# Performance work log

Hardware: AMD Instinct MI355X
Metric: run time of the kernel (lower is better)

Reference implementation:

```python
import jax, jax.numpy as jnp
import numpy as np

B, S, D = 4, 2048, 1024
H, K = 16, 64
EPS = 1e-3  # Keras LayerNormalization default epsilon


def setup_inputs() -> dict:
    key = jax.random.key(0)
    ks = jax.random.split(key, 11)
    s = 0.02
    return {
        "x":  jax.random.normal(ks[0], (B, S, D), jnp.float32),
        "Wq": jax.random.normal(ks[1], (D, H, K), jnp.float32) * s,
        "bq": jnp.zeros((H, K), jnp.float32),
        "Wk": jax.random.normal(ks[2], (D, H, K), jnp.float32) * s,
        "bk": jnp.zeros((H, K), jnp.float32),
        "Wv": jax.random.normal(ks[3], (D, H, K), jnp.float32) * s,
        "bv": jnp.zeros((H, K), jnp.float32),
        "Wo": jax.random.normal(ks[4], (H, K, D), jnp.float32) * s,
        "bo": jnp.zeros((D,), jnp.float32),
        "gamma": jnp.ones((D,), jnp.float32),
        "beta":  jnp.zeros((D,), jnp.float32),
    }


def reference(x, Wq, bq, Wk, bk, Wv, bv, Wo, bo, gamma, beta):
    # QKV projections (Keras MHA einsum form): [B,S,D] -> [B,S,H,K]
    q = jnp.einsum("bsd,dhk->bshk", x, Wq) + bq
    k = jnp.einsum("bsd,dhk->bshk", x, Wk) + bk
    v = jnp.einsum("bsd,dhk->bshk", x, Wv) + bv
    scale = 1.0 / jnp.sqrt(jnp.asarray(K, x.dtype))
    scores = jnp.einsum("bqhk,bshk->bhqs", q, k) * scale  # [B,H,S,S]
    attn = jax.nn.softmax(scores, axis=-1)
    ctx = jnp.einsum("bhqs,bshk->bqhk", attn, v)           # [B,S,H,K]
    attn_out = jnp.einsum("bqhk,hkd->bqd", ctx, Wo) + bo   # [B,S,D]
    # residual + LayerNorm (over last axis)
    y = x + attn_out
    mu = jnp.mean(y, axis=-1, keepdims=True)
    var = jnp.mean(jnp.square(y - mu), axis=-1, keepdims=True)
    return (y - mu) * jax.lax.rsqrt(var + EPS) * gamma + beta
```

## Files before the change

kernel.cpp:

```cpp
#include <hip/hip_runtime.h>

typedef float f32x4 __attribute__((ext_vector_type(4)));
typedef float f32x16 __attribute__((ext_vector_type(16)));
typedef __bf16 bf16x8 __attribute__((ext_vector_type(8)));
typedef __bf16 bf16x4 __attribute__((ext_vector_type(4)));
typedef __bf16 bf16x2 __attribute__((ext_vector_type(2)));
typedef unsigned short us4 __attribute__((ext_vector_type(4)));

#define DEV __device__ __forceinline__

DEV unsigned short f2bf(float f) {
  union { float f; unsigned int u; } v; v.f = f;
  unsigned int u = v.u;
  return (unsigned short)((u + 0x7FFFu + ((u >> 16) & 1u)) >> 16);
}

typedef const __attribute__((address_space(1))) void* gvp;
typedef __attribute__((address_space(3))) void* lvp;

DEV void gll16(const void* g, void* l) {
  __builtin_amdgcn_global_load_lds((gvp)g, (lvp)l, 16, 0, 0);
}

DEV float fexp2(float x) { return __builtin_amdgcn_exp2f(x); }

DEV void plswap(unsigned& a, unsigned& b) {
  asm("v_permlane32_swap_b32 %0, %1" : "+v"(a), "+v"(b));
}
DEV float xhalf_sum(float v) {
  union { float f; unsigned u; } a, b;
  a.f = v; b.f = v;
  plswap(a.u, b.u);
  return a.f + b.f;
}

__global__ void k_pre(const float* __restrict__ x, unsigned short* __restrict__ xb,
                      const float* __restrict__ w0, const float* __restrict__ w1,
                      const float* __restrict__ w2, const float* __restrict__ w3,
                      unsigned short* __restrict__ o0, unsigned short* __restrict__ o1,
                      unsigned short* __restrict__ o2, unsigned short* __restrict__ o3) {
  __shared__ float tile[32][33];
  const int bid = blockIdx.x;
  const int tid = threadIdx.x;
  if (bid < 8192) {
    int i = bid * 256 + tid;
    float4 v = ((const float4*)x)[i];
    us4 o = { f2bf(v.x), f2bf(v.y), f2bf(v.z), f2bf(v.w) };
    ((us4*)xb)[i] = o;
    return;
  }
  int t = bid - 8192;
  const int z = t >> 10;
  t &= 1023;
  const float* in = (z == 0) ? w0 : (z == 1) ? w1 : (z == 2) ? w2 : w3;
  unsigned short* out = (z == 0) ? o0 : (z == 1) ? o1 : (z == 2) ? o2 : o3;
  const int bx = (t & 31) * 32, by = (t >> 5) * 32;
  const int tx = tid & 31, ty = tid >> 5;
#pragma unroll
  for (int r = 0; r < 4; ++r)
    tile[ty + r * 8][tx] = in[(size_t)(by + ty + r * 8) * 1024 + bx + tx];
  __syncthreads();
#pragma unroll
  for (int r = 0; r < 4; ++r)
    out[(size_t)(bx + ty + r * 8) * 1024 + by + tx] = f2bf(tile[tx][ty + r * 8]);
}

__global__ void k_gemm_qkv(const unsigned short* __restrict__ xb,
                           const unsigned short* __restrict__ wqt,
                           const unsigned short* __restrict__ wkt,
                           const unsigned short* __restrict__ wvt,
                           const float* __restrict__ bq, const float* __restrict__ bk,
                           const float* __restrict__ bv,
                           unsigned short* __restrict__ qb, unsigned short* __restrict__ kb,
                           unsigned short* __restrict__ vtb) {
  __shared__ unsigned short SM[2][128 * 64];
  unsigned short* As = SM[0];
  unsigned short* Bs = SM[1];
  const int tid = threadIdx.x;
  const int lane = tid & 63;
  const int wave = tid >> 6;
  const int l15 = lane & 15;
  const int lq  = lane >> 4;
  const int wm = wave >> 1, wn = wave & 1;
  const int z = blockIdx.z;

  const unsigned short* A;
  const unsigned short* Bt;
  int mbase, nbase;
  if (z == 2) { A = wvt; Bt = xb; mbase = blockIdx.y * 128; nbase = blockIdx.x * 128; }
  else        { A = xb; Bt = z ? wkt : wqt; mbase = blockIdx.x * 128; nbase = blockIdx.y * 128; }

  f32x4 acc[4][4] = {};

  for (int kt = 0; kt < 1024; kt += 64) {
    __syncthreads();
#pragma unroll
    for (int c = 0; c < 4; ++c) {
      int e = (c * 256 + tid) * 8;
      int row = e >> 6;
      int o2 = (e * 2) ^ ((row & 7) << 4);
      int col = (o2 >> 1) & 63;
      gll16(A + (size_t)(mbase + row) * 1024 + kt + col,
            As + (c * 256 + (tid & ~63)) * 8);
      gll16(Bt + (size_t)(nbase + row) * 1024 + kt + col,
            Bs + (c * 256 + (tid & ~63)) * 8);
    }
    __syncthreads();
#pragma unroll
    for (int ks = 0; ks < 2; ++ks) {
      bf16x8 af[4], bfv[4];
#pragma unroll
      for (int i = 0; i < 4; ++i) {
        int row = wm * 64 + i * 16 + l15;
        int off = row * 128 + ((((ks << 2) | lq) ^ (row & 7)) << 4);
        af[i] = *(const bf16x8*)((const char*)As + off);
      }
#pragma unroll
      for (int j = 0; j < 4; ++j) {
        int row = wn * 64 + j * 16 + l15;
        int off = row * 128 + ((((ks << 2) | lq) ^ (row & 7)) << 4);
        bfv[j] = *(const bf16x8*)((const char*)Bs + off);
      }
#pragma unroll
      for (int i = 0; i < 4; ++i)
#pragma unroll
        for (int j = 0; j < 4; ++j)
          acc[i][j] = __builtin_amdgcn_mfma_f32_16x16x32_bf16(bfv[j], af[i], acc[i][j], 0, 0, 0);
    }
  }

  const float scale = (z == 0) ? 0.18033688011112042f : 1.0f;
  const float* bias = (z == 0) ? bq : (z == 1) ? bk : bv;
  unsigned short* outp = (z == 0) ? qb : (z == 1) ? kb : vtb;

  float4 bj[4];
  if (z < 2) {
#pragma unroll
    for (int j = 0; j < 4; ++j)
      bj[j] = *(const float4*)&bias[nbase + wn * 64 + j * 16 + lq * 4];
  }

  __syncthreads();
  char* T = (char*)SM;
#pragma unroll
  for (int i = 0; i < 4; ++i) {
    const int miL = wm * 64 + i * 16 + l15;
    const int sw = (miL & 7) << 4;
    const float bm = (z == 2) ? bias[mbase + miL] : 0.f;
#pragma unroll
    for (int j = 0; j < 4; ++j) {
      const int nj2 = (wn * 64 + j * 16 + lq * 4) * 2;
      bf16x4 p;
#pragma unroll
      for (int r = 0; r < 4; ++r) {
        float v = acc[i][j][r];
        v = (z < 2) ? (v + ((const float*)&bj[j])[r]) * scale : (v + bm);
        p[r] = (__bf16)v;
      }
      *(bf16x4*)(T + miL * 256 + (nj2 ^ sw)) = p;
    }
  }
  __syncthreads();

#pragma unroll
  for (int c = 0; c < 8; ++c) {
    const int lin = c * 256 + tid;
    const int row = lin >> 4;
    const int s16 = lin & 15;
    bf16x8 vv = *(const bf16x8*)(T + row * 256 + ((s16 * 16) ^ ((row & 7) << 4)));
    const int mi = mbase + row;
    const int nj = nbase + s16 * 8;
    size_t gaddr;
    if (z < 2) {
      gaddr = (((size_t)((mi >> 11) * 16 + (nj >> 6)) * 2048 + (mi & 2047)) << 6) + (nj & 63);
    } else {
      gaddr = ((size_t)(((nj >> 11) * 16 + (mi >> 6)) * 64 + (mi & 63))) * 2048 + (nj & 2047);
    }
    *(bf16x8*)(outp + gaddr) = vv;
  }
}

__global__ void k_gemm_out(const unsigned short* __restrict__ A,
                           const unsigned short* __restrict__ Bt,
                           const float* __restrict__ bias,
                           unsigned short* __restrict__ yb,
                           const unsigned short* __restrict__ xres) {
  __shared__ unsigned short SM[2][128 * 64];
  unsigned short* As = SM[0];
  unsigned short* Bs = SM[1];
  const int tid = threadIdx.x;
  const int lane = tid & 63;
  const int wave = tid >> 6;
  const int l15 = lane & 15;
  const int lq  = lane >> 4;
  const int wm = wave >> 1, wn = wave & 1;
  const int mbase = blockIdx.x * 128;
  const int nbase = blockIdx.y * 128;

  f32x4 acc[4][4] = {};

  for (int kt = 0; kt < 1024; kt += 64) {
    __syncthreads();
#pragma unroll
    for (int c = 0; c < 4; ++c) {
      int e = (c * 256 + tid) * 8;
      int row = e >> 6;
      int o2 = (e * 2) ^ ((row & 7) << 4);
      int col = (o2 >> 1) & 63;
      gll16(A + (size_t)(mbase + row) * 1024 + kt + col,
            As + (c * 256 + (tid & ~63)) * 8);
      gll16(Bt + (size_t)(nbase + row) * 1024 + kt + col,
            Bs + (c * 256 + (tid & ~63)) * 8);
    }
    __syncthreads();
#pragma unroll
    for (int ks = 0; ks < 2; ++ks) {
      bf16x8 af[4], bfv[4];
#pragma unroll
      for (int i = 0; i < 4; ++i) {
        int row = wm * 64 + i * 16 + l15;
        int off = row * 128 + ((((ks << 2) | lq) ^ (row & 7)) << 4);
        af[i] = *(const bf16x8*)((const char*)As + off);
      }
#pragma unroll
      for (int j = 0; j < 4; ++j) {
        int row = wn * 64 + j * 16 + l15;
        int off = row * 128 + ((((ks << 2) | lq) ^ (row & 7)) << 4);
        bfv[j] = *(const bf16x8*)((const char*)Bs + off);
      }
#pragma unroll
      for (int i = 0; i < 4; ++i)
#pragma unroll
        for (int j = 0; j < 4; ++j)
          acc[i][j] = __builtin_amdgcn_mfma_f32_16x16x32_bf16(bfv[j], af[i], acc[i][j], 0, 0, 0);
    }
  }

  float4 bj[4];
#pragma unroll
  for (int j = 0; j < 4; ++j)
    bj[j] = *(const float4*)&bias[nbase + wn * 64 + j * 16 + lq * 4];

  __syncthreads();
  char* T = (char*)SM;
#pragma unroll
  for (int i = 0; i < 4; ++i) {
    const int miL = wm * 64 + i * 16 + l15;
    const int sw = (miL & 7) << 4;
#pragma unroll
    for (int j = 0; j < 4; ++j) {
      const int nj2 = (wn * 64 + j * 16 + lq * 4) * 2;
      bf16x4 p;
#pragma unroll
      for (int r = 0; r < 4; ++r)
        p[r] = (__bf16)(acc[i][j][r] + ((const float*)&bj[j])[r]);
      *(bf16x4*)(T + miL * 256 + (nj2 ^ sw)) = p;
    }
  }
  __syncthreads();

#pragma unroll
  for (int c = 0; c < 8; ++c) {
    const int lin = c * 256 + tid;
    const int row = lin >> 4;
    const int s16 = lin & 15;
    bf16x8 vv = *(const bf16x8*)(T + row * 256 + ((s16 * 16) ^ ((row & 7) << 4)));
    const size_t g = (size_t)(mbase + row) * 1024 + nbase + s16 * 8;
    bf16x8 xv = *(const bf16x8*)(xres + g);
    bf16x8 ov;
#pragma unroll
    for (int e = 0; e < 8; ++e)
      ov[e] = (__bf16)((float)vv[e] + (float)xv[e]);
    *(bf16x8*)(yb + g) = ov;
  }
}

__global__ __launch_bounds__(256, 4) void k_attn(const unsigned short* __restrict__ q,
                       const unsigned short* __restrict__ k,
                       const unsigned short* __restrict__ vt,
                       unsigned short* __restrict__ ctx) {
  __shared__ unsigned short KV[2][2][64 * 64];

  const int tid = threadIdx.x;
  const int lane = tid & 63;
  const int wave = tid >> 6;
  const int l31 = lane & 31;
  const int l5 = lane >> 5;
  const int prl = l31 >> 1;
  const int b3  = (l31 & 1) << 3;

  const int bid = blockIdx.x;
  const int swz = (bid & 7) * 128 + (bid >> 3);
  const int bh = swz >> 4;
  const int qtile = swz & 15;
  const int qbase = qtile * 128;
  const size_t sl = (size_t)bh << 17;

  const int qrow = qbase + wave * 32 + l31;
  bf16x8 qreg[4];
#pragma unroll
  for (int ds = 0; ds < 4; ++ds)
    qreg[ds] = *(const bf16x8*)(q + sl + (size_t)qrow * 64 + ds * 16 + l5 * 8);

#define STAGE_KV(BUF, TT) do {                                                 \
    const int kvb_ = (TT) * 64;                                                \
    _Pragma("unroll")                                                          \
    for (int c = 0; c < 2; ++c) {                                              \
      int ci = c * 256 + tid;                                                  \
      int pr_ = ci >> 4;                                                       \
      int u_ = (ci & 15) ^ (pr_ & 15);                                         \
      int lrow_ = pr_ * 2 + (u_ >> 3);                                         \
      int lc_ = u_ & 7;                                                        \
      gll16(k + sl + (size_t)(kvb_ + lrow_) * 64 + lc_ * 8,                    \
            KV[BUF][0] + (c * 256 + (tid & ~63)) * 8);                         \
      gll16(vt + sl + (size_t)lrow_ * 2048 + kvb_ + lc_ * 8,                   \
            KV[BUF][1] + (c * 256 + (tid & ~63)) * 8);                         \
    }                                                                          \
  } while (0)

  STAGE_KV(0, 0);
  __syncthreads();

  f32x16 acc0 = {}, acc1 = {};
  float lrow = 0.f;

  for (int t = 0; t < 32; ++t) {
    const int cur = t & 1;
    if (t < 31) STAGE_KV(cur ^ 1, t + 1);

    const char* Ksc = (const char*)KV[cur][0];
    const char* Vtc = (const char*)KV[cur][1];

    bf16x8 kf0[4], kf1[4];
#pragma unroll
    for (int ds = 0; ds < 4; ++ds) {
      int sc = (b3 | (2 * ds + l5)) ^ prl;
      kf0[ds] = *(const bf16x8*)(Ksc + prl * 256 + sc * 16);
      kf1[ds] = *(const bf16x8*)(Ksc + 4096 + prl * 256 + sc * 16);
    }
    f32x16 s0 = {}, s1 = {};
    __builtin_amdgcn_s_setprio(1);
#pragma unroll
    for (int ds = 0; ds < 4; ++ds)
      s0 = __builtin_amdgcn_mfma_f32_32x32x16_bf16(kf0[ds], qreg[ds], s0, 0, 0, 0);
#pragma unroll
    for (int ds = 0; ds < 4; ++ds)
      s1 = __builtin_amdgcn_mfma_f32_32x32x16_bf16(kf1[ds], qreg[ds], s1, 0, 0, 0);
    __builtin_amdgcn_s_setprio(0);
    __builtin_amdgcn_sched_barrier(0);

    unsigned pk0[8], pk1[8];
    float r0s = 0.f, r1s = 0.f, r2s = 0.f, r3s = 0.f;
#pragma unroll
    for (int m = 0; m < 8; ++m) {
      float a0 = fexp2(s0[2 * m]), a1 = fexp2(s0[2 * m + 1]);
      float b0 = fexp2(s1[2 * m]), b1 = fexp2(s1[2 * m + 1]);
      r0s += a0; r1s += a1; r2s += b0; r3s += b1;
      union { bf16x2 v; unsigned u; } ua, ub;
      ua.v = bf16x2{ (__bf16)a0, (__bf16)a1 };
      ub.v = bf16x2{ (__bf16)b0, (__bf16)b1 };
      pk0[m] = ua.u; pk1[m] = ub.u;
    }
    lrow += (r0s + r1s) + (r2s + r3s);
    __builtin_amdgcn_sched_barrier(0);

    bf16x8 av0[4], av1[4];
#pragma unroll
    for (int kvg = 0; kvg < 4; ++kvg) {
      int sc = (b3 | (2 * kvg + l5)) ^ prl;
      av0[kvg] = *(const bf16x8*)(Vtc + prl * 256 + sc * 16);
      av1[kvg] = *(const bf16x8*)(Vtc + 4096 + prl * 256 + sc * 16);
    }
    __builtin_amdgcn_s_setprio(1);
#pragma unroll
    for (int kvh = 0; kvh < 2; ++kvh) {
      unsigned* pk = kvh ? pk1 : pk0;
#pragma unroll
      for (int g = 0; g < 2; ++g) {
        unsigned a0_ = pk[4 * g],     b0_ = pk[4 * g + 2];
        unsigned a1_ = pk[4 * g + 1], b1_ = pk[4 * g + 3];
        plswap(a0_, b0_);
        plswap(a1_, b1_);
        union { unsigned u[4]; bf16x8 v; } pf;
        pf.u[0] = a0_; pf.u[1] = a1_; pf.u[2] = b0_; pf.u[3] = b1_;
        const int kvg = 2 * kvh + g;
        acc0 = __builtin_amdgcn_mfma_f32_32x32x16_bf16(av0[kvg], pf.v, acc0, 0, 0, 0);
        acc1 = __builtin_amdgcn_mfma_f32_32x32x16_bf16(av1[kvg], pf.v, acc1, 0, 0, 0);
      }
    }
    __builtin_amdgcn_s_setprio(0);

    __syncthreads();
  }

  const float inv = 1.f / xhalf_sum(lrow);

  unsigned short* TR = (unsigned short*)KV;
  const int qloc = wave * 32 + l31;
  const int swq = (qloc & 7) << 4;
#pragma unroll
  for (int dh = 0; dh < 2; ++dh) {
    const f32x16& ac = dh ? acc1 : acc0;
#pragma unroll
    for (int g3 = 0; g3 < 4; ++g3) {
      bf16x4 o4 = { (__bf16)(ac[4 * g3] * inv), (__bf16)(ac[4 * g3 + 1] * inv),
                    (__bf16)(ac[4 * g3 + 2] * inv), (__bf16)(ac[4 * g3 + 3] * inv) };
      *(bf16x4*)((char*)TR + qloc * 128 + ((dh * 64 + g3 * 16 + l5 * 8) ^ swq)) = o4;
    }
  }
  __syncthreads();

  const int b = bh >> 4, h = bh & 15;
  {
    int row = tid >> 1, half = tid & 1;
    int sw = (row & 7) << 4;
    unsigned short* gdst = ctx + (size_t)(b * 2048 + qbase + row) * 1024 + h * 64 + half * 32;
#pragma unroll
    for (int i = 0; i < 4; ++i) {
      bf16x8 vv = *(const bf16x8*)((const char*)TR + row * 128 + ((half * 64 + i * 16) ^ sw));
      *(bf16x8*)(gdst + i * 8) = vv;
    }
  }
#undef STAGE_KV
}

__global__ void k_ln(const unsigned short* __restrict__ y, const float* __restrict__ gamma,
                     const float* __restrict__ beta, float* __restrict__ out) {
  const int row = blockIdx.x;
  const int tid = threadIdx.x;
  const bf16x4 v4 = *(const bf16x4*)(y + (size_t)row * 1024 + tid * 4);
  float v0 = (float)v4[0], v1 = (float)v4[1], v2 = (float)v4[2], v3 = (float)v4[3];
  float sum = v0 + v1 + v2 + v3;
  float sq = v0 * v0 + v1 * v1 + v2 * v2 + v3 * v3;
#pragma unroll
  for (int m = 1; m <= 32; m <<= 1) {
    sum += __shfl_xor(sum, m);
    sq  += __shfl_xor(sq, m);
  }
  __shared__ float s1[4], s2[4];
  const int wv = tid >> 6, lane = tid & 63;
  if (lane == 0) { s1[wv] = sum; s2[wv] = sq; }
  __syncthreads();
  sum = s1[0] + s1[1] + s1[2] + s1[3];
  sq  = s2[0] + s2[1] + s2[2] + s2[3];
  const float mu = sum * (1.f / 1024.f);
  const float rs = rsqrtf(sq * (1.f / 1024.f) - mu * mu + 1e-3f);
  const float4 g  = ((const float4*)gamma)[tid];
  const float4 bb = ((const float4*)beta)[tid];
  float4 o;
  o.x = (v0 - mu) * rs * g.x + bb.x;
  o.y = (v1 - mu) * rs * g.y + bb.y;
  o.z = (v2 - mu) * rs * g.z + bb.z;
  o.w = (v3 - mu) * rs * g.w + bb.w;
  ((float4*)(out + (size_t)row * 1024))[tid] = o;
}

extern "C" void kernel_launch(void* const* d_in, const int* in_sizes, int n_in,
                              void* d_out, int out_size, void* d_ws, size_t ws_size,
                              hipStream_t stream) {
  const float* x  = (const float*)d_in[0];
  const float* Wq = (const float*)d_in[1];
  const float* bq = (const float*)d_in[2];
  const float* Wk = (const float*)d_in[3];
  const float* bk = (const float*)d_in[4];
  const float* Wv = (const float*)d_in[5];
  const float* bv = (const float*)d_in[6];
  const float* Wo = (const float*)d_in[7];
  const float* bo = (const float*)d_in[8];
  const float* gamma = (const float*)d_in[9];
  const float* beta  = (const float*)d_in[10];
  float* out = (float*)d_out;

  char* ws = (char*)d_ws;
  const size_t MB = 1024 * 1024;
  unsigned short* xb  = (unsigned short*)(ws);
  unsigned short* wqt = (unsigned short*)(ws + 16 * MB);
  unsigned short* wkt = (unsigned short*)(ws + 18 * MB);
  unsigned short* wvt = (unsigned short*)(ws + 20 * MB);
  unsigned short* wot = (unsigned short*)(ws + 22 * MB);
  unsigned short* qb  = (unsigned short*)(ws + 24 * MB);
  unsigned short* kb  = (unsigned short*)(ws + 40 * MB);
  unsigned short* vtb = (unsigned short*)(ws + 56 * MB);
  unsigned short* ctx = (unsigned short*)(ws + 72 * MB);
  unsigned short* yb  = (unsigned short*)(ws + 24 * MB);

  k_pre<<<12288, 256, 0, stream>>>(x, xb, Wq, Wk, Wv, Wo, wqt, wkt, wvt, wot);

  k_gemm_qkv<<<dim3(64, 8, 3), 256, 0, stream>>>(xb, wqt, wkt, wvt, bq, bk, bv, qb, kb, vtb);

  k_attn<<<1024, 256, 0, stream>>>(qb, kb, vtb, ctx);

  k_gemm_out<<<dim3(64, 8), 256, 0, stream>>>(ctx, wot, bo, yb, xb);

  k_ln<<<8192, 256, 0, stream>>>(yb, gamma, beta, out);
  (void)in_sizes; (void)n_in; (void)out_size; (void)ws_size;
}
```

Before: 175.2 us.

## Split Q/K projection into 256x256 eight-wave pipelined GEMM, keep separate V kernel

Replaces the combined QKV GEMM with a dedicated Q/K kernel using 256x256 tiles, 512 threads and a hand-scheduled double-buffered global_load_lds pipeline. It relies on explicit vmcnt waits, sched barriers and setprio around the MFMA bursts. The Wq and Wk weights are treated as one contiguous 2048-wide B matrix. V is computed by a separate smaller kernel using the old tiling. The aim is higher data reuse per tile and overlapping loads with MFMA work. The cost is fragile manual wait counts and only one block per CU.

After: 179.0 us. +2.2%, slower.

```diff
diff --git a/kernel.cpp b/kernel.cpp
--- a/kernel.cpp
+++ b/kernel.cpp
@@ -65,30 +65,181 @@
     out[(size_t)(bx + ty + r * 8) * 1024 + by + tx] = f2bf(tile[tx][ty + r * 8]);
 }
 
-__global__ void k_gemm_qkv(const unsigned short* __restrict__ xb,
-                           const unsigned short* __restrict__ wqt,
-                           const unsigned short* __restrict__ wkt,
-                           const unsigned short* __restrict__ wvt,
-                           const float* __restrict__ bq, const float* __restrict__ bk,
-                           const float* __restrict__ bv,
-                           unsigned short* __restrict__ qb, unsigned short* __restrict__ kb,
-                           unsigned short* __restrict__ vtb) {
-  __shared__ unsigned short SM[2][128 * 64];
-  unsigned short* As = SM[0];
-  unsigned short* Bs = SM[1];
+__global__ __launch_bounds__(512, 1) void k_gemm8_qk(
+    const unsigned short* __restrict__ A,
+    const unsigned short* __restrict__ Bt,
+    const float* __restrict__ bq, const float* __restrict__ bk,
+    unsigned short* __restrict__ qb, unsigned short* __restrict__ kb) {
+  __shared__ unsigned short SM[65536];
+  const int tid = threadIdx.x;
+  const int lane = tid & 63;
+  const int wave = tid >> 6;
+  const int l15 = lane & 15;
+  const int lq = lane >> 4;
+  const int wm = wave >> 2;
+  const int wn = wave & 3;
+
+  const int lin = blockIdx.x;
+  const int swz = (lin & 7) * 32 + (lin >> 3);
+  const int mt = swz & 31, nt = swz >> 5;
+  const int mbase = mt * 256, nbase = nt * 256;
+  const int z = nt >> 2;
+
+  const int sgrow = tid >> 3;
+  const int sgo2 = ((tid & 7) * 16) ^ ((sgrow & 7) << 4);
+  const int sgcol = sgo2 >> 1;
+  const int sdst = (tid & ~63) * 8;
+
+#define SQA(PAR, HALF, S, T) \
+  gll16(A + (size_t)(mbase + (HALF) * 128 + (S) * 64 + sgrow) * 1024 + (T) * 64 + sgcol, \
+        SM + (PAR) * 16384 + (HALF) * 8192 + (S) * 4096 + sdst)
+#define SQB(PAR, HALF, S, T) \
+  gll16(Bt + (size_t)(nbase + (HALF) * 128 + (S) * 64 + sgrow) * 1024 + (T) * 64 + sgcol, \
+        SM + 32768 + (PAR) * 16384 + (HALF) * 8192 + (S) * 4096 + sdst)
+#define SLOT_Aq(PAR, S, T) do { SQA(PAR, 0, S, T); SQA(PAR, 1, S, T); } while (0)
+#define SLOT_Bq(PAR, S, T) do { SQB(PAR, 0, S, T); SQB(PAR, 1, S, T); } while (0)
+
+  f32x4 acc[8][4] = {};
+  bf16x8 afr[4][2], bfr[2][2];
+
+  const char* Ab0 = (const char*)(SM + wm * 8192);
+  const char* Ab1 = (const char*)(SM + 16384 + wm * 8192);
+  const char* Bb0 = (const char*)(SM + 32768 + (wn >> 1) * 8192);
+  const char* Bb1 = (const char*)(SM + 49152 + (wn >> 1) * 8192);
+
+#define PHASE(ABASE, BBASE, MH, NH, LOADA, WAITSTMT, STAGESTMT) do {           \
+    WAITSTMT;                                                                  \
+    __builtin_amdgcn_s_barrier();                                              \
+    __builtin_amdgcn_sched_barrier(0);                                         \
+    if (LOADA) {                                                               \
+      _Pragma("unroll")                                                        \
+      for (int i = 0; i < 4; ++i) {                                            \
+        int lr = (MH) * 64 + i * 16 + l15;                                     \
+        _Pragma("unroll")                                                      \
+        for (int ks = 0; ks < 2; ++ks)                                         \
+          afr[i][ks] = *(const bf16x8*)((ABASE) + lr * 128 +                   \
+                        ((((ks << 2) | lq) ^ (lr & 7)) << 4));                 \
+      }                                                                        \
+    }                                                                          \
+    _Pragma("unroll")                                                          \
+    for (int j = 0; j < 2; ++j) {                                              \
+      int br = (wn & 1) * 64 + (NH) * 32 + j * 16 + l15;                       \
+      _Pragma("unroll")                                                        \
+      for (int ks = 0; ks < 2; ++ks)                                           \
+        bfr[j][ks] = *(const bf16x8*)((BBASE) + br * 128 +                     \
+                      ((((ks << 2) | lq) ^ (br & 7)) << 4));                   \
+    }                                                                          \
+    STAGESTMT;                                                                 \
+    asm volatile("s_waitcnt lgkmcnt(0)" ::: "memory");                         \
+    __builtin_amdgcn_sched_barrier(0);                                         \
+    __builtin_amdgcn_s_setprio(1);                                             \
+    _Pragma("unroll")                                                          \
+    for (int i = 0; i < 4; ++i)                                                \
+      _Pragma("unroll")                                                        \
+      for (int j = 0; j < 2; ++j)                                              \
+        _Pragma("unroll")                                                      \
+        for (int ks = 0; ks < 2; ++ks)                                         \
+          acc[(MH) * 4 + i][(NH) * 2 + j] =                                    \
+            __builtin_amdgcn_mfma_f32_16x16x32_bf16(bfr[j][ks], afr[i][ks],    \
+                acc[(MH) * 4 + i][(NH) * 2 + j], 0, 0, 0);                     \
+    __builtin_amdgcn_s_setprio(0);                                             \
+  } while (0)
+
+#define VM4 asm volatile("s_waitcnt vmcnt(4)" ::: "memory")
+#define VM6 asm volatile("s_waitcnt vmcnt(6)" ::: "memory")
+#define VM8 asm volatile("s_waitcnt vmcnt(8)" ::: "memory")
+#define VM0 asm volatile("s_waitcnt vmcnt(0)" ::: "memory")
+#define NOW ((void)0)
+
+  SLOT_Aq(0, 0, 0); SLOT_Bq(0, 0, 0); SLOT_Aq(0, 1, 0); SLOT_Bq(0, 1, 0);
+  SLOT_Aq(1, 0, 1); SLOT_Bq(1, 0, 1);
+
+  for (int J = 0; J < 7; ++J) {
+    const int Tb = 2 * J + 1, Tc = 2 * J + 2, Td = 2 * J + 3;
+    PHASE(Ab0, Bb0, 0, 0, true,  VM4, SLOT_Aq(1, 1, Tb));
+    PHASE(Ab0, Bb0, 0, 1, false, NOW, SLOT_Bq(1, 1, Tb));
+    PHASE(Ab0, Bb0, 1, 0, true,  NOW, SLOT_Aq(0, 0, Tc));
+    PHASE(Ab0, Bb0, 1, 1, false, NOW, SLOT_Bq(0, 0, Tc));
+    PHASE(Ab1, Bb1, 0, 0, true,  VM8, SLOT_Aq(0, 1, Tc));
+    PHASE(Ab1, Bb1, 0, 1, false, VM6, SLOT_Bq(0, 1, Tc));
+    PHASE(Ab1, Bb1, 1, 0, true,  NOW, SLOT_Aq(1, 0, Td));
+    PHASE(Ab1, Bb1, 1, 1, false, NOW, SLOT_Bq(1, 0, Td));
+  }
+  PHASE(Ab0, Bb0, 0, 0, true,  VM4, SLOT_Aq(1, 1, 15));
+  PHASE(Ab0, Bb0, 0, 1, false, NOW, SLOT_Bq(1, 1, 15));
+  PHASE(Ab0, Bb0, 1, 0, true,  NOW, NOW);
+  PHASE(Ab0, Bb0, 1, 1, false, NOW, NOW);
+  PHASE(Ab1, Bb1, 0, 0, true,  VM4, NOW);
+  PHASE(Ab1, Bb1, 0, 1, false, VM0, NOW);
+  PHASE(Ab1, Bb1, 1, 0, true,  NOW, NOW);
+  PHASE(Ab1, Bb1, 1, 1, false, NOW, NOW);
+
+  const float scale = z ? 1.0f : 0.18033688011112042f;
+  const float* bias = z ? bk : bq;
+  unsigned short* outp = z ? kb : qb;
+  const int nnb = (nbase & 1023) + wn * 64;
+
+  float4 bj[4];
+#pragma unroll
+  for (int fj = 0; fj < 4; ++fj)
+    bj[fj] = *(const float4*)&bias[nnb + (fj >> 1) * 32 + (fj & 1) * 16 + lq * 4];
+
+  __syncthreads();
+  char* T = (char*)SM;
+#pragma unroll
+  for (int fi = 0; fi < 8; ++fi) {
+    const int row = wm * 128 + fi * 16 + l15;
+    const int sw = (row & 7) << 4;
+#pragma unroll
+    for (int fj = 0; fj < 4; ++fj) {
+      const int cb = wn * 128 + (fj >> 1) * 64 + (fj & 1) * 32 + lq * 8;
+      bf16x4 p;
+#pragma unroll
+      for (int r = 0; r < 4; ++r)
+        p[r] = (__bf16)((acc[fi][fj][r] + ((const float*)&bj[fj])[r]) * scale);
+      *(bf16x4*)(T + row * 512 + (cb ^ sw)) = p;
+    }
+  }
+  __syncthreads();
+
+#pragma unroll
+  for (int c = 0; c < 16; ++c) {
+    const int lin2 = c * 512 + tid;
+    const int row = lin2 >> 5;
+    const int ch = lin2 & 31;
+    bf16x8 vv = *(const bf16x8*)(T + row * 512 + ((ch * 16) ^ ((row & 7) << 4)));
+    const int mi = mbase + row;
+    const int nn = (nbase & 1023) + ch * 8;
+    const int b = mi >> 11, s = mi & 2047, h = nn >> 6, kk = nn & 63;
+    *(bf16x8*)(outp + (((size_t)(b * 16 + h) * 2048 + s) << 6) + kk) = vv;
+  }
+#undef SQA
+#undef SQB
+#undef SLOT_Aq
+#undef SLOT_Bq
+#undef PHASE
+#undef VM4
+#undef VM6
+#undef VM8
+#undef VM0
+#undef NOW
+}
+
+__global__ void k_gemm_vt(const unsigned short* __restrict__ A,
+                          const unsigned short* __restrict__ Bt,
+                          const float* __restrict__ bias,
+                          unsigned short* __restrict__ vtb) {
+  __shared__ unsigned short SMv[2][128 * 64];
+  unsigned short* As = SMv[0];
+  unsigned short* Bs = SMv[1];
   const int tid = threadIdx.x;
   const int lane = tid & 63;
   const int wave = tid >> 6;
   const int l15 = lane & 15;
   const int lq  = lane >> 4;
   const int wm = wave >> 1, wn = wave & 1;
-  const int z = blockIdx.z;
-
-  const unsigned short* A;
-  const unsigned short* Bt;
-  int mbase, nbase;
-  if (z == 2) { A = wvt; Bt = xb; mbase = blockIdx.y * 128; nbase = blockIdx.x * 128; }
-  else        { A = xb; Bt = z ? wkt : wqt; mbase = blockIdx.x * 128; nbase = blockIdx.y * 128; }
+  const int mbase = blockIdx.y * 128;
+  const int nbase = blockIdx.x * 128;
 
   f32x4 acc[4][4] = {};
 
@@ -129,34 +280,20 @@
     }
   }
 
-  const float scale = (z == 0) ? 0.18033688011112042f : 1.0f;
-  const float* bias = (z == 0) ? bq : (z == 1) ? bk : bv;
-  unsigned short* outp = (z == 0) ? qb : (z == 1) ? kb : vtb;
-
-  float4 bj[4];
-  if (z < 2) {
-#pragma unroll
-    for (int j = 0; j < 4; ++j)
-      bj[j] = *(const float4*)&bias[nbase + wn * 64 + j * 16 + lq * 4];
-  }
-
-  __syncthreads();
-  char* T = (char*)SM;
+  __syncthreads();
+  char* T = (char*)SMv;
 #pragma unroll
   for (int i = 0; i < 4; ++i) {
     const int miL = wm * 64 + i * 16 + l15;
     const int sw = (miL & 7) << 4;
-    const float bm = (z == 2) ? bias[mbase + miL] : 0.f;
+    const float bm = bias[mbase + miL];
 #pragma unroll
     for (int j = 0; j < 4; ++j) {
       const int nj2 = (wn * 64 + j * 16 + lq * 4) * 2;
       bf16x4 p;
 #pragma unroll
-      for (int r = 0; r < 4; ++r) {
-        float v = acc[i][j][r];
-        v = (z < 2) ? (v + ((const float*)&bj[j])[r]) * scale : (v + bm);
-        p[r] = (__bf16)v;
-      }
+      for (int r = 0; r < 4; ++r)
+        p[r] = (__bf16)(acc[i][j][r] + bm);
       *(bf16x4*)(T + miL * 256 + (nj2 ^ sw)) = p;
     }
   }
@@ -170,13 +307,8 @@
     bf16x8 vv = *(const bf16x8*)(T + row * 256 + ((s16 * 16) ^ ((row & 7) << 4)));
     const int mi = mbase + row;
     const int nj = nbase + s16 * 8;
-    size_t gaddr;
-    if (z < 2) {
-      gaddr = (((size_t)((mi >> 11) * 16 + (nj >> 6)) * 2048 + (mi & 2047)) << 6) + (nj & 63);
-    } else {
-      gaddr = ((size_t)(((nj >> 11) * 16 + (mi >> 6)) * 64 + (mi & 63))) * 2048 + (nj & 2047);
-    }
-    *(bf16x8*)(outp + gaddr) = vv;
+    size_t gaddr = ((size_t)(((nj >> 11) * 16 + (mi >> 6)) * 64 + (mi & 63))) * 2048 + (nj & 2047);
+    *(bf16x8*)(vtb + gaddr) = vv;
   }
 }
 
@@ -185,9 +317,9 @@
                            const float* __restrict__ bias,
                            unsigned short* __restrict__ yb,
                            const unsigned short* __restrict__ xres) {
-  __shared__ unsigned short SM[2][128 * 64];
-  unsigned short* As = SM[0];
-  unsigned short* Bs = SM[1];
+  __shared__ unsigned short SMo[2][128 * 64];
+  unsigned short* As = SMo[0];
+  unsigned short* Bs = SMo[1];
   const int tid = threadIdx.x;
   const int lane = tid & 63;
   const int wave = tid >> 6;
@@ -242,7 +374,7 @@
     bj[j] = *(const float4*)&bias[nbase + wn * 64 + j * 16 + lq * 4];
 
   __syncthreads();
-  char* T = (char*)SM;
+  char* T = (char*)SMo;
 #pragma unroll
   for (int i = 0; i < 4; ++i) {
     const int miL = wm * 64 + i * 16 + l15;
@@ -486,7 +618,8 @@
 
   k_pre<<<12288, 256, 0, stream>>>(x, xb, Wq, Wk, Wv, Wo, wqt, wkt, wvt, wot);
 
-  k_gemm_qkv<<<dim3(64, 8, 3), 256, 0, stream>>>(xb, wqt, wkt, wvt, bq, bk, bv, qb, kb, vtb);
+  k_gemm8_qk<<<256, 512, 0, stream>>>(xb, wqt, bq, bk, qb, kb);
+  k_gemm_vt<<<dim3(64, 8), 256, 0, stream>>>(wvt, xb, bv, vtb);
 
   k_attn<<<1024, 256, 0, stream>>>(qb, kb, vtb, ctx);
 
```

## Split K/V staging in attention with triple-buffered K and one barrier per step

Applied to the files above, without the earlier changes.

The attention kernel now stages K and V tiles separately, with three K buffers and two V buffers in shared memory. The next V tile is issued right after the QK^T MFMAs and the K tile two steps ahead is issued at the end of the iteration. The trailing __syncthreads is replaced by a partial vmcnt wait plus a barrier at the top of each step. This aims to hide global-to-LDS load latency and cut barrier stalls. In exchange, shared memory grows from 32 KB to 40 KB per block, which may limit occupancy, and the final iterations issue redundant loads.

New measurement: 183.8 us. 4.9% more time.

```diff
diff --git a/kernel.cpp b/kernel.cpp
--- a/kernel.cpp
+++ b/kernel.cpp
@@ -185,9 +185,9 @@
                            const float* __restrict__ bias,
                            unsigned short* __restrict__ yb,
                            const unsigned short* __restrict__ xres) {
-  __shared__ unsigned short SM[2][128 * 64];
-  unsigned short* As = SM[0];
-  unsigned short* Bs = SM[1];
+  __shared__ unsigned short SMo[2][128 * 64];
+  unsigned short* As = SMo[0];
+  unsigned short* Bs = SMo[1];
   const int tid = threadIdx.x;
   const int lane = tid & 63;
   const int wave = tid >> 6;
@@ -242,7 +242,7 @@
     bj[j] = *(const float4*)&bias[nbase + wn * 64 + j * 16 + lq * 4];
 
   __syncthreads();
-  char* T = (char*)SM;
+  char* T = (char*)SMo;
 #pragma unroll
   for (int i = 0; i < 4; ++i) {
     const int miL = wm * 64 + i * 16 + l15;
@@ -279,7 +279,8 @@
                        const unsigned short* __restrict__ k,
                        const unsigned short* __restrict__ vt,
                        unsigned short* __restrict__ ctx) {
-  __shared__ unsigned short KV[2][2][64 * 64];
+  __shared__ unsigned short KL[3][64 * 64];
+  __shared__ unsigned short VL[2][64 * 64];
 
   const int tid = threadIdx.x;
   const int lane = tid & 63;
@@ -302,7 +303,7 @@
   for (int ds = 0; ds < 4; ++ds)
     qreg[ds] = *(const bf16x8*)(q + sl + (size_t)qrow * 64 + ds * 16 + l5 * 8);
 
-#define STAGE_KV(BUF, TT) do {                                                 \
+#define STAGE_K(DST, TT) do {                                                  \
     const int kvb_ = (TT) * 64;                                                \
     _Pragma("unroll")                                                          \
     for (int c = 0; c < 2; ++c) {                                              \
@@ -312,24 +313,36 @@
       int lrow_ = pr_ * 2 + (u_ >> 3);                                         \
       int lc_ = u_ & 7;                                                        \
       gll16(k + sl + (size_t)(kvb_ + lrow_) * 64 + lc_ * 8,                    \
-            KV[BUF][0] + (c * 256 + (tid & ~63)) * 8);                         \
-      gll16(vt + sl + (size_t)lrow_ * 2048 + kvb_ + lc_ * 8,                   \
-            KV[BUF][1] + (c * 256 + (tid & ~63)) * 8);                         \
+            (DST) + (c * 256 + (tid & ~63)) * 8);                              \
     }                                                                          \
   } while (0)
-
-  STAGE_KV(0, 0);
-  __syncthreads();
+#define STAGE_V(DST, TT) do {                                                  \
+    const int kvb_ = (TT) * 64;                                                \
+    _Pragma("unroll")                                                          \
+    for (int c = 0; c < 2; ++c) {                                              \
+      int ci = c * 256 + tid;                                                  \
+      int pr_ = ci >> 4;                                                       \
+      int u_ = (ci & 15) ^ (pr_ & 15);                                         \
+      int lrow_ = pr_ * 2 + (u_ >> 3);                                         \
+      int lc_ = u_ & 7;                                                        \
+      gll16(vt + sl + (size_t)lrow_ * 2048 + kvb_ + lc_ * 8,                   \
+            (DST) + (c * 256 + (tid & ~63)) * 8);                              \
+    }                                                                          \
+  } while (0)
+
+  STAGE_K(KL[0], 0);
+  STAGE_V(VL[0], 0);
+  STAGE_K(KL[1], 1);
 
   f32x16 acc0 = {}, acc1 = {};
   float lrow = 0.f;
 
   for (int t = 0; t < 32; ++t) {
-    const int cur = t & 1;
-    if (t < 31) STAGE_KV(cur ^ 1, t + 1);
-
-    const char* Ksc = (const char*)KV[cur][0];
-    const char* Vtc = (const char*)KV[cur][1];
+    asm volatile("s_waitcnt vmcnt(2)" ::: "memory");
+    __builtin_amdgcn_s_barrier();
+
+    const char* Ksc = (const char*)KL[t % 3];
+    const char* Vtc = (const char*)VL[t & 1];
 
     bf16x8 kf0[4], kf1[4];
 #pragma unroll
@@ -347,6 +360,11 @@
     for (int ds = 0; ds < 4; ++ds)
       s1 = __builtin_amdgcn_mfma_f32_32x32x16_bf16(kf1[ds], qreg[ds], s1, 0, 0, 0);
     __builtin_amdgcn_s_setprio(0);
+
+    {
+      const int tv = (t + 1 < 32) ? t + 1 : 31;
+      STAGE_V(VL[(t + 1) & 1], tv);
+    }
     __builtin_amdgcn_sched_barrier(0);
 
     unsigned pk0[8], pk1[8];
@@ -390,12 +408,16 @@
     }
     __builtin_amdgcn_s_setprio(0);
 
-    __syncthreads();
+    {
+      const int tk = (t + 2 < 32) ? t + 2 : 31;
+      STAGE_K(KL[(t + 2) % 3], tk);
+    }
   }
 
   const float inv = 1.f / xhalf_sum(lrow);
 
-  unsigned short* TR = (unsigned short*)KV;
+  __syncthreads();
+  unsigned short* TR = (unsigned short*)KL;
   const int qloc = wave * 32 + l31;
   const int swq = (qloc & 7) << 4;
 #pragma unroll
@@ -421,7 +443,8 @@
       *(bf16x8*)(gdst + i * 8) = vv;
     }
   }
-#undef STAGE_KV
+#undef STAGE_K
+#undef STAGE_V
 }
 
 __global__ void k_ln(const unsigned short* __restrict__ y, const float* __restrict__ gamma,
```
